# Kernel optimization log

Measured on AMD Instinct MI355X. Metric: run time of the kernel, lower is better.

Reference implementation:

```python
import jax, jax.numpy as jnp
import numpy as np

N, E, G = 20000, 320000, 16
IN, HID, OUT, HEADS = 256, 64, 256, 4
D0 = HID * HEADS  # 256, output dim of layer 0 (concat)


def _p(key, shape, scale=0.05):
    return (jax.random.normal(key, shape, dtype=jnp.float32) * scale)


def setup_inputs() -> dict:
    key = jax.random.key(0)
    ks = jax.random.split(key, 24)
    x = jax.random.normal(ks[0], (N, IN), dtype=jnp.float32)
    edge_index = jax.random.randint(ks[1], (2, E), 0, N, dtype=jnp.int64)
    batch = jnp.sort(jax.random.randint(ks[2], (N,), 0, G, dtype=jnp.int64))
    d = {"x": x, "edge_index": edge_index, "batch": batch}
    # Layer 0: TransformerConv(256 -> 64, heads=4, concat=True, beta=True)
    d["Wq0"] = _p(ks[3], (IN, D0)); d["bq0"] = jnp.zeros((D0,), jnp.float32)
    d["Wk0"] = _p(ks[4], (IN, D0)); d["bk0"] = jnp.zeros((D0,), jnp.float32)
    d["Wv0"] = _p(ks[5], (IN, D0)); d["bv0"] = jnp.zeros((D0,), jnp.float32)
    d["Ws0"] = _p(ks[6], (IN, D0)); d["bs0"] = jnp.zeros((D0,), jnp.float32)
    d["Wb0"] = _p(ks[7], (3 * D0, 1))
    d["g0"] = jnp.ones((D0,), jnp.float32); d["b0"] = jnp.zeros((D0,), jnp.float32)
    # Layer 1: TransformerConv(256 -> 256, heads=1, concat=False, beta=True)
    d["Wq1"] = _p(ks[8], (D0, OUT)); d["bq1"] = jnp.zeros((OUT,), jnp.float32)
    d["Wk1"] = _p(ks[9], (D0, OUT)); d["bk1"] = jnp.zeros((OUT,), jnp.float32)
    d["Wv1"] = _p(ks[10], (D0, OUT)); d["bv1"] = jnp.zeros((OUT,), jnp.float32)
    d["Ws1"] = _p(ks[11], (D0, OUT)); d["bs1"] = jnp.zeros((OUT,), jnp.float32)
    d["Wb1"] = _p(ks[12], (3 * OUT, 1))
    d["g1"] = jnp.ones((OUT,), jnp.float32); d["b1"] = jnp.zeros((OUT,), jnp.float32)
    return d


def _transformer_conv(x, src, dst, Wq, bq, Wk, bk, Wv, bv, Ws, bs, Wb, H, C, concat):
    n = x.shape[0]
    q = (x @ Wq + bq).reshape(n, H, C)
    k = (x @ Wk + bk).reshape(n, H, C)
    v = (x @ Wv + bv).reshape(n, H, C)
    # per-edge attention logits [E, H]
    alpha = (q[dst] * k[src]).sum(-1) / jnp.sqrt(jnp.asarray(C, jnp.float32))
    # segment softmax over incoming edges of each dst node
    m = jax.ops.segment_max(alpha, dst, num_segments=n)  # [N, H]
    a = jnp.exp(alpha - m[dst])
    s = jax.ops.segment_sum(a, dst, num_segments=n)  # [N, H]
    a = a / s[dst]
    out = jax.ops.segment_sum(a[:, :, None] * v[src], dst, num_segments=n)  # [N,H,C]
    out = out.reshape(n, H * C) if concat else out.mean(axis=1)
    # beta-gated skip connection
    r = x @ Ws + bs
    g = jax.nn.sigmoid(jnp.concatenate([out, r, out - r], axis=-1) @ Wb)  # [N,1]
    return g * r + (1.0 - g) * out


def _layer_norm(x, g, b, eps=1e-5):
    mu = x.mean(-1, keepdims=True)
    var = x.var(-1, keepdims=True)
    return (x - mu) * jax.lax.rsqrt(var + eps) * g + b


def reference(x, edge_index, batch,
              Wq0, bq0, Wk0, bk0, Wv0, bv0, Ws0, bs0, Wb0, g0, b0,
              Wq1, bq1, Wk1, bk1, Wv1, bv1, Ws1, bs1, Wb1, g1, b1):
    src, dst = edge_index[0], edge_index[1]
    h = _transformer_conv(x, src, dst, Wq0, bq0, Wk0, bk0, Wv0, bv0, Ws0, bs0, Wb0, HEADS, HID, True)
    h = jax.nn.relu(_layer_norm(h, g0, b0))  # dropout is identity at inference
    h = _transformer_conv(h, src, dst, Wq1, bq1, Wk1, bk1, Wv1, bv1, Ws1, bs1, Wb1, 1, OUT, False)
    h = _layer_norm(h, g1, b1)
    # global mean pool over graphs
    sums = jax.ops.segment_sum(h, batch, num_segments=G)
    counts = jax.ops.segment_sum(jnp.ones((h.shape[0],), h.dtype), batch, num_segments=G)
    return sums / jnp.maximum(counts, 1.0)[:, None]
```

## Files before the change

### kernel.cpp

```cpp
#include <hip/hip_runtime.h>
#include <hip/hip_bf16.h>


#define DEVFN static __device__ __forceinline__

typedef __attribute__((ext_vector_type(4))) float f32x4;
typedef __attribute__((ext_vector_type(2))) float f32x2;
typedef __attribute__((ext_vector_type(8))) short bf16x8;

DEVFN float bfu2f(unsigned short u) {
    union { unsigned int i; float f; } t; t.i = ((unsigned)u) << 16; return t.f;
}
DEVFN float4 ldb4(const __hip_bfloat16* p) {
    ushort4 u = *reinterpret_cast<const ushort4*>(p);
    return make_float4(bfu2f(u.x), bfu2f(u.y), bfu2f(u.z), bfu2f(u.w));
}
DEVFN unsigned short f2bu(float f) {
    __hip_bfloat16 b = __float2bfloat16(f);
    return __builtin_bit_cast(unsigned short, b);
}
DEVFN void stb4(__hip_bfloat16* p, float4 v) {
    ushort4 u;
    u.x = f2bu(v.x); u.y = f2bu(v.y); u.z = f2bu(v.z); u.w = f2bu(v.w);
    *reinterpret_cast<ushort4*>(p) = u;
}
DEVFN float4 f8x4_to_f4(unsigned u) {
    const f32x2 lo = __builtin_amdgcn_cvt_pk_f32_fp8((int)u, false);
    const f32x2 hi = __builtin_amdgcn_cvt_pk_f32_fp8((int)u, true);
    return make_float4(lo.x, lo.y, hi.x, hi.y);
}

DEVFN float dot16(const float* q, uint4 u) {
    const float4 f0 = f8x4_to_f4(u.x);
    const float4 f1 = f8x4_to_f4(u.y);
    const float4 f2 = f8x4_to_f4(u.z);
    const float4 f3 = f8x4_to_f4(u.w);
    float p;
    p = q[0] * f0.x;            p = fmaf(q[1],  f0.y, p);
    p = fmaf(q[2],  f0.z, p);   p = fmaf(q[3],  f0.w, p);
    p = fmaf(q[4],  f1.x, p);   p = fmaf(q[5],  f1.y, p);
    p = fmaf(q[6],  f1.z, p);   p = fmaf(q[7],  f1.w, p);
    p = fmaf(q[8],  f2.x, p);   p = fmaf(q[9],  f2.y, p);
    p = fmaf(q[10], f2.z, p);   p = fmaf(q[11], f2.w, p);
    p = fmaf(q[12], f3.x, p);   p = fmaf(q[13], f3.y, p);
    p = fmaf(q[14], f3.z, p);   p = fmaf(q[15], f3.w, p);
    return p;
}
DEVFN void accum16(float* acc, uint4 u, float a) {
    const float4 f0 = f8x4_to_f4(u.x);
    const float4 f1 = f8x4_to_f4(u.y);
    const float4 f2 = f8x4_to_f4(u.z);
    const float4 f3 = f8x4_to_f4(u.w);
    acc[0]  = fmaf(a, f0.x, acc[0]);  acc[1]  = fmaf(a, f0.y, acc[1]);
    acc[2]  = fmaf(a, f0.z, acc[2]);  acc[3]  = fmaf(a, f0.w, acc[3]);
    acc[4]  = fmaf(a, f1.x, acc[4]);  acc[5]  = fmaf(a, f1.y, acc[5]);
    acc[6]  = fmaf(a, f1.z, acc[6]);  acc[7]  = fmaf(a, f1.w, acc[7]);
    acc[8]  = fmaf(a, f2.x, acc[8]);  acc[9]  = fmaf(a, f2.y, acc[9]);
    acc[10] = fmaf(a, f2.z, acc[10]); acc[11] = fmaf(a, f2.w, acc[11]);
    acc[12] = fmaf(a, f3.x, acc[12]); acc[13] = fmaf(a, f3.y, acc[13]);
    acc[14] = fmaf(a, f3.z, acc[14]); acc[15] = fmaf(a, f3.w, acc[15]);
}

__global__ __launch_bounds__(256)
void f2b_kernel(const float* __restrict__ in, __hip_bfloat16* __restrict__ out, int n4)
{
    const int i = blockIdx.x * 256 + threadIdx.x;
    if (i >= n4) return;
    const float4 v = *reinterpret_cast<const float4*>(in + (size_t)i * 4);
    stb4(out + (size_t)i * 4, v);
}

__global__ __launch_bounds__(256)
void wconv_kernel(const float* __restrict__ W0, const float* __restrict__ W1,
                  const float* __restrict__ W2, const float* __restrict__ W3,
                  const float* __restrict__ W4, const float* __restrict__ W5,
                  const float* __restrict__ W6, const float* __restrict__ W7,
                  __hip_bfloat16* __restrict__ Wt)
{
    const float* W;
    switch (blockIdx.y) {
        case 0: W = W0; break; case 1: W = W1; break;
        case 2: W = W2; break; case 3: W = W3; break;
        case 4: W = W4; break; case 5: W = W5; break;
        case 6: W = W6; break; default: W = W7; break;
    }
    const int k = blockIdx.x;
    const int c = threadIdx.x;
    Wt[(size_t)blockIdx.y * 65536 + (size_t)c * 256 + k] =
        __float2bfloat16(W[(size_t)k * 256 + c]);
}

#define SWZ(r, kb) ((r) * 256 + ((kb) ^ (((r) & 7) << 4)))
#define TSTRIDE 272

__global__ __launch_bounds__(256)
void gemm_mfma_kernel(const __hip_bfloat16* __restrict__ A, int M,
                      const __hip_bfloat16* __restrict__ Wt,
                      const float* __restrict__ b0, const float* __restrict__ b1,
                      const float* __restrict__ b2, const float* __restrict__ b3,
                      void* __restrict__ O0, void* __restrict__ O1,
                      void* __restrict__ O2, void* __restrict__ O3,
                      int s0, int s1, int s2, int s3,
                      int f0, int f1, int f2, int f3)
{
    const int q8   = gridDim.x >> 3;
    const int wgid = (blockIdx.x & 7) * q8 + (blockIdx.x >> 3);
    const int rowblk = wgid >> 3;
    const int rem    = wgid & 7;
    const int colblk = rem >> 2;
    const int z      = rem & 3;

    const float* bias; void* O; int rs, isf8;
    switch (z) {
        case 0:  bias = b0; O = O0; rs = s0; isf8 = f0; break;
        case 1:  bias = b1; O = O1; rs = s1; isf8 = f1; break;
        case 2:  bias = b2; O = O2; rs = s2; isf8 = f2; break;
        default: bias = b3; O = O3; rs = s3; isf8 = f3; break;
    }
    const __hip_bfloat16* Wz = Wt + (size_t)z * 65536;

    __shared__ char Sh[2 * 128 * 256];
    char* As = Sh;
    char* Bs = Sh + 128 * 256;

    const int tid  = threadIdx.x;
    const int row0 = rowblk * 128;
    const int col0 = colblk * 128;
    const int wid  = tid >> 6, lane = tid & 63;
    const int wr   = wid >> 1, wc = wid & 1;
    const int lrow = lane & 15, kg = lane >> 4;

    const int chunk = tid & 15;
    const int rsub  = tid >> 4;

    f32x4 acc[4][4] = {};

    for (int k0 = 0; k0 < 256; k0 += 128) {
        #pragma unroll
        for (int p = 0; p < 8; ++p) {
            const int r  = p * 16 + rsub;
            const int gr = row0 + r;
            ulonglong2 av = {0ull, 0ull};
            if (gr < M)
                av = *reinterpret_cast<const ulonglong2*>(A + (size_t)gr * 256 + k0 + chunk * 8);
            *reinterpret_cast<ulonglong2*>(As + SWZ(r, chunk * 16)) = av;

            const ulonglong2 bv = *reinterpret_cast<const ulonglong2*>(
                Wz + (size_t)(col0 + r) * 256 + k0 + chunk * 8);
            *reinterpret_cast<ulonglong2*>(Bs + SWZ(r, chunk * 16)) = bv;
        }
        __syncthreads();

        #pragma unroll
        for (int kk = 0; kk < 128; kk += 32) {
            const int kbyte = kk * 2 + kg * 16;
            bf16x8 af[4], bfr[4];
            #pragma unroll
            for (int m = 0; m < 4; ++m) {
                const int r = wr * 64 + m * 16 + lrow;
                af[m] = *reinterpret_cast<const bf16x8*>(As + SWZ(r, kbyte));
            }
            #pragma unroll
            for (int n = 0; n < 4; ++n) {
                const int c = wc * 64 + n * 16 + lrow;
                bfr[n] = *reinterpret_cast<const bf16x8*>(Bs + SWZ(c, kbyte));
            }
            #pragma unroll
            for (int m = 0; m < 4; ++m)
                #pragma unroll
                for (int n = 0; n < 4; ++n)
                    acc[m][n] = __builtin_amdgcn_mfma_f32_16x16x32_bf16(
                        af[m], bfr[n], acc[m][n], 0, 0, 0);
        }
        __syncthreads();
    }

    #pragma unroll
    for (int m = 0; m < 4; ++m) {
        #pragma unroll
        for (int j = 0; j < 4; ++j) {
            const int rr = wr * 64 + m * 16 + kg * 4 + j;
            #pragma unroll
            for (int n = 0; n < 4; ++n) {
                const int cc = wc * 64 + n * 16 + lrow;
                const float v = acc[m][n][j] + bias[col0 + cc];
                *reinterpret_cast<unsigned short*>(Sh + rr * TSTRIDE + cc * 2) = f2bu(v);
            }
        }
    }
    __syncthreads();

    const int row  = tid >> 1;
    const int half = tid & 1;
    const int grow = row0 + row;
    if (grow >= M) return;
    const char* src = Sh + row * TSTRIDE + half * 128;

    if (isf8) {
        unsigned char* dst = (unsigned char*)O + (size_t)grow * rs + col0 + half * 64;
        #pragma unroll
        for (int i2 = 0; i2 < 4; ++i2) {
            uint4 w;
            unsigned tmp[4];
            #pragma unroll
            for (int c8 = 0; c8 < 2; ++c8) {
                const bf16x8 e = *reinterpret_cast<const bf16x8*>(src + (i2 * 2 + c8) * 16);
                const int p0 = __builtin_amdgcn_cvt_pk_fp8_f32(
                    bfu2f((unsigned short)e[0]), bfu2f((unsigned short)e[1]), 0, false);
                const int p1 = __builtin_amdgcn_cvt_pk_fp8_f32(
                    bfu2f((unsigned short)e[2]), bfu2f((unsigned short)e[3]), 0, false);
                const int p2 = __builtin_amdgcn_cvt_pk_fp8_f32(
                    bfu2f((unsigned short)e[4]), bfu2f((unsigned short)e[5]), 0, false);
                const int p3 = __builtin_amdgcn_cvt_pk_fp8_f32(
                    bfu2f((unsigned short)e[6]), bfu2f((unsigned short)e[7]), 0, false);
                tmp[c8 * 2 + 0] = (unsigned)(p0 & 0xFFFF) | ((unsigned)(p1 & 0xFFFF) << 16);
                tmp[c8 * 2 + 1] = (unsigned)(p2 & 0xFFFF) | ((unsigned)(p3 & 0xFFFF) << 16);
            }
            w.x = tmp[0]; w.y = tmp[1]; w.z = tmp[2]; w.w = tmp[3];
            *reinterpret_cast<uint4*>(dst + i2 * 16) = w;
        }
    } else {
        char* dst = (char*)((__hip_bfloat16*)O + (size_t)grow * rs + col0 + half * 64);
        #pragma unroll
        for (int i = 0; i < 8; ++i)
            *reinterpret_cast<ulonglong2*>(dst + i * 16) =
                *reinterpret_cast<const ulonglong2*>(src + i * 16);
    }
}

__global__ __launch_bounds__(256)
void hist_kernel(const int* __restrict__ ei, int E, int* __restrict__ deg)
{
    const int e = blockIdx.x * 256 + threadIdx.x;
    if (e < E) atomicAdd(&deg[ei[E + e]], 1);
}

__global__ __launch_bounds__(256)
void gcount_kernel(const int* __restrict__ batch, int N, int* __restrict__ gcount)
{
    __shared__ int h[16];
    if (threadIdx.x < 16) h[threadIdx.x] = 0;
    __syncthreads();
    const int n = blockIdx.x * 256 + threadIdx.x;
    if (n < N) atomicAdd(&h[batch[n]], 1);
    __syncthreads();
    if (threadIdx.x < 16 && h[threadIdx.x] != 0)
        atomicAdd(&gcount[threadIdx.x], h[threadIdx.x]);
}

__global__ __launch_bounds__(64)
void gstart_kernel(const int* __restrict__ gcount, int* __restrict__ gstart)
{
    if (threadIdx.x == 0) {
        int o = 0;
        for (int g = 0; g < 16; ++g) { gstart[g] = o; o += gcount[g]; }
        gstart[16] = o;
    }
}

__global__ __launch_bounds__(1024)
void scan_kernel(const int* __restrict__ deg, int* __restrict__ row_start, int n)
{
    __shared__ int wsum[16];
    __shared__ int wincl[16];
    const int tid  = threadIdx.x;
    const int w    = tid >> 6;
    const int lane = tid & 63;
    if (tid == 0) row_start[0] = 0;
    int offset = 0;
    for (int base = 0; base < n; base += 1024) {
        const int idx = base + tid;
        int s = (idx < n) ? deg[idx] : 0;
        #pragma unroll
        for (int d = 1; d < 64; d <<= 1) {
            const int t = __shfl_up(s, d, 64);
            if (lane >= d) s += t;
        }
        if (lane == 63) wsum[w] = s;
        __syncthreads();
        if (tid < 16) {
            int si = wsum[tid];
            #pragma unroll
            for (int d = 1; d < 16; d <<= 1) {
                const int u = __shfl_up(si, d, 64);
                if (tid >= d) si += u;
            }
            wincl[tid] = si;
        }
        __syncthreads();
        const int woff = (w > 0) ? wincl[w - 1] : 0;
        if (idx < n) row_start[idx + 1] = offset + woff + s;
        offset += wincl[15];
        __syncthreads();
    }
}

__global__ __launch_bounds__(256)
void fill_kernel(const int* __restrict__ ei, int E,
                 const int* __restrict__ row_start,
                 int* __restrict__ cursor, int* __restrict__ csr_src)
{
    const int e = blockIdx.x * 256 + threadIdx.x;
    if (e >= E) return;
    const int s = ei[e];
    const int d = ei[E + e];
    const int pos = atomicAdd(&cursor[d], 1);
    csr_src[row_start[d] + pos] = s;
}

template <int NSH, bool RELU, bool OUTB>
__global__ __launch_bounds__(256)
void attn_kernel(const __hip_bfloat16* __restrict__ Q,
                 const unsigned char* __restrict__ KV,
                 const __hip_bfloat16* __restrict__ R,
                 const float* __restrict__ Wb, const float* __restrict__ lng,
                 const float* __restrict__ lnb,
                 const int* __restrict__ row_start, const int* __restrict__ csr_src,
                 __hip_bfloat16* __restrict__ outb, float* __restrict__ outf,
                 int N, float scale)
{
    const int wv   = threadIdx.x >> 6;
    const int lane = threadIdx.x & 63;
    const int g    = lane >> 4;
    const int s    = lane & 15;
    const int node = blockIdx.x * 4 + wv;
    if (node >= N) return;

    float q[16];
    {
        const bf16x8 a = *reinterpret_cast<const bf16x8*>(Q + (size_t)node * 256 + s * 16);
        const bf16x8 b = *reinterpret_cast<const bf16x8*>(Q + (size_t)node * 256 + s * 16 + 8);
        #pragma unroll
        for (int j = 0; j < 8; ++j) {
            q[j]     = bfu2f((unsigned short)a[j]);
            q[8 + j] = bfu2f((unsigned short)b[j]);
        }
    }

    const int beg = row_start[node];
    const int end = row_start[node + 1];

    float acc[16] = {};
    float ssum = 0.f;

    int i = beg + g;
    for (; i + 4 < end; i += 8) {
        const int sa = csr_src[i];
        const int sb = csr_src[i + 4];
        const uint4 ka = *reinterpret_cast<const uint4*>(KV + (size_t)sa * 512 + s * 16);
        const uint4 va = *reinterpret_cast<const uint4*>(KV + (size_t)sa * 512 + 256 + s * 16);
        const uint4 kb = *reinterpret_cast<const uint4*>(KV + (size_t)sb * 512 + s * 16);
        const uint4 vb = *reinterpret_cast<const uint4*>(KV + (size_t)sb * 512 + 256 + s * 16);
        float pa = dot16(q, ka);
        float pb = dot16(q, kb);
        #pragma unroll
        for (int m = 1; m < (1 << NSH); m <<= 1) {
            pa += __shfl_xor(pa, m, 64);
            pb += __shfl_xor(pb, m, 64);
        }
        const float aa = __expf(pa * scale);
        const float ab = __expf(pb * scale);
        ssum += aa + ab;
        accum16(acc, va, aa);
        accum16(acc, vb, ab);
    }
    if (i < end) {
        const int sa = csr_src[i];
        const uint4 ka = *reinterpret_cast<const uint4*>(KV + (size_t)sa * 512 + s * 16);
        const uint4 va = *reinterpret_cast<const uint4*>(KV + (size_t)sa * 512 + 256 + s * 16);
        float pa = dot16(q, ka);
        #pragma unroll
        for (int m = 1; m < (1 << NSH); m <<= 1) pa += __shfl_xor(pa, m, 64);
        const float aa = __expf(pa * scale);
        ssum += aa;
        accum16(acc, va, aa);
    }

    ssum += __shfl_xor(ssum, 16, 64);
    ssum += __shfl_xor(ssum, 32, 64);
    #pragma unroll
    for (int j = 0; j < 16; ++j) {
        acc[j] += __shfl_xor(acc[j], 16, 64);
        acc[j] += __shfl_xor(acc[j], 32, 64);
    }

    if (g != 0) return;

    const float is = (ssum > 0.f) ? 1.f / ssum : 0.f;
    float o[16];
    #pragma unroll
    for (int j = 0; j < 16; ++j) o[j] = acc[j] * is;

    float r[16];
    {
        const bf16x8 a = *reinterpret_cast<const bf16x8*>(R + (size_t)node * 256 + s * 16);
        const bf16x8 b = *reinterpret_cast<const bf16x8*>(R + (size_t)node * 256 + s * 16 + 8);
        #pragma unroll
        for (int j = 0; j < 8; ++j) {
            r[j]     = bfu2f((unsigned short)a[j]);
            r[8 + j] = bfu2f((unsigned short)b[j]);
        }
    }

    float z = 0.f;
    #pragma unroll
    for (int j = 0; j < 16; ++j) {
        const int d = s * 16 + j;
        z += o[j] * Wb[d] + r[j] * Wb[256 + d] + (o[j] - r[j]) * Wb[512 + d];
    }
    #pragma unroll
    for (int m = 1; m < 16; m <<= 1) z += __shfl_xor(z, m, 64);
    const float gg = 1.f / (1.f + __expf(-z));

    float h[16];
    float s1 = 0.f, s2 = 0.f;
    #pragma unroll
    for (int j = 0; j < 16; ++j) {
        h[j] = gg * r[j] + (1.f - gg) * o[j];
        s1 += h[j];
        s2 += h[j] * h[j];
    }
    #pragma unroll
    for (int m = 1; m < 16; m <<= 1) {
        s1 += __shfl_xor(s1, m, 64);
        s2 += __shfl_xor(s2, m, 64);
    }
    const float mu  = s1 * (1.f / 256.f);
    const float var = s2 * (1.f / 256.f) - mu * mu;
    const float inv = rsqrtf(var + 1e-5f);

    #pragma unroll
    for (int j = 0; j < 16; ++j) {
        const int d = s * 16 + j;
        h[j] = (h[j] - mu) * inv * lng[d] + lnb[d];
        if (RELU) h[j] = fmaxf(h[j], 0.f);
    }

    if (OUTB) {
        __hip_bfloat16* dst = outb + (size_t)node * 256 + s * 16;
        stb4(dst,      make_float4(h[0],  h[1],  h[2],  h[3]));
        stb4(dst + 4,  make_float4(h[4],  h[5],  h[6],  h[7]));
        stb4(dst + 8,  make_float4(h[8],  h[9],  h[10], h[11]));
        stb4(dst + 12, make_float4(h[12], h[13], h[14], h[15]));
    } else {
        float* dst = outf + (size_t)node * 256 + s * 16;
        #pragma unroll
        for (int c4 = 0; c4 < 4; ++c4)
            *reinterpret_cast<float4*>(dst + c4 * 4) =
                make_float4(h[c4 * 4], h[c4 * 4 + 1], h[c4 * 4 + 2], h[c4 * 4 + 3]);
    }
}

__global__ __launch_bounds__(256)
void pool_partial_kernel(const float* __restrict__ h, const int* __restrict__ gstart,
                         float* __restrict__ partial)
{
    const int s    = blockIdx.x;
    const int g    = blockIdx.y;
    const int tid  = threadIdx.x;
    const int quad = tid & 63;
    const int sub  = tid >> 6;

    const int beg = gstart[g];
    const int cnt = gstart[g + 1] - beg;

    f32x4 acc = {0.f, 0.f, 0.f, 0.f};
    for (int i = s * 4 + sub; i < cnt; i += 64) {
        const f32x4 v = *reinterpret_cast<const f32x4*>(
            h + (size_t)(beg + i) * 256 + quad * 4);
        acc += v;
    }

    __shared__ f32x4 sh[4][64];
    sh[sub][quad] = acc;
    __syncthreads();
    if (sub == 0) {
        const f32x4 r = sh[0][quad] + sh[1][quad] + sh[2][quad] + sh[3][quad];
        *reinterpret_cast<f32x4*>(partial + ((size_t)(g * 16 + s) * 64 + quad) * 4) = r;
    }
}

__global__ __launch_bounds__(256)
void pool_final_kernel(const float* __restrict__ partial, const int* __restrict__ gcount,
                       float* __restrict__ out)
{
    const int g = blockIdx.x;
    const int d = threadIdx.x;
    float sum = 0.f;
    #pragma unroll
    for (int s = 0; s < 16; ++s)
        sum += partial[(size_t)(g * 16 + s) * 256 + d];
    out[(size_t)g * 256 + d] = sum / (float)max(gcount[g], 1);
}

extern "C" void kernel_launch(void* const* d_in, const int* in_sizes, int n_in,
                              void* d_out, int out_size, void* d_ws, size_t ws_size,
                              hipStream_t stream)
{
    const float* x     = (const float*)d_in[0];
    const int*   ei    = (const int*)d_in[1];
    const int*   batch = (const int*)d_in[2];
    const float* Wq0 = (const float*)d_in[3];  const float* bq0 = (const float*)d_in[4];
    const float* Wk0 = (const float*)d_in[5];  const float* bk0 = (const float*)d_in[6];
    const float* Wv0 = (const float*)d_in[7];  const float* bv0 = (const float*)d_in[8];
    const float* Ws0 = (const float*)d_in[9];  const float* bs0 = (const float*)d_in[10];
    const float* Wb0 = (const float*)d_in[11];
    const float* g0  = (const float*)d_in[12]; const float* b0  = (const float*)d_in[13];
    const float* Wq1 = (const float*)d_in[14]; const float* bq1 = (const float*)d_in[15];
    const float* Wk1 = (const float*)d_in[16]; const float* bk1 = (const float*)d_in[17];
    const float* Wv1 = (const float*)d_in[18]; const float* bv1 = (const float*)d_in[19];
    const float* Ws1 = (const float*)d_in[20]; const float* bs1 = (const float*)d_in[21];
    const float* Wb1 = (const float*)d_in[22];
    const float* g1  = (const float*)d_in[23]; const float* b1  = (const float*)d_in[24];

    const int N = in_sizes[0] / 256;
    const int E = in_sizes[1] / 2;
    const int G = 16;
    const size_t NM = (size_t)N * 256;

    __hip_bfloat16* bws = (__hip_bfloat16*)d_ws;
    __hip_bfloat16* xb  = bws;
    __hip_bfloat16* qb  = xb  + NM;
    __hip_bfloat16* rb  = qb  + NM;
    __hip_bfloat16* h0b = rb  + NM;
    __hip_bfloat16* wt  = h0b + NM;
    unsigned char* kvb  = (unsigned char*)(wt + 8 * 65536);
    float* h1f     = (float*)(kvb + (size_t)N * 512);
    float* partial = h1f + NM;
    int* deg       = (int*)(partial + 16 * 16 * 256);
    int* row_start = deg + N;
    int* cursor    = row_start + N + 1;
    int* gcount    = cursor + N;
    int* gstart    = gcount + G;
    int* csr_src   = gstart + 17;

    const size_t zbytes = ((size_t)N + (N + 1) + N + G + 17) * sizeof(int);
    hipMemsetAsync(deg, 0, zbytes, stream);

    const int eb = (E + 255) / 256;
    const int nb = (N + 255) / 256;

    f2b_kernel<<<(int)((NM / 4 + 255) / 256), 256, 0, stream>>>(x, xb, (int)(NM / 4));
    wconv_kernel<<<dim3(256, 8), 256, 0, stream>>>(Wq0, Wk0, Wv0, Ws0,
                                                   Wq1, Wk1, Wv1, Ws1, wt);

    hist_kernel<<<eb, 256, 0, stream>>>(ei, E, deg);
    gcount_kernel<<<nb, 256, 0, stream>>>(batch, N, gcount);
    gstart_kernel<<<1, 64, 0, stream>>>(gcount, gstart);
    scan_kernel<<<1, 1024, 0, stream>>>(deg, row_start, N);
    fill_kernel<<<eb, 256, 0, stream>>>(ei, E, row_start, cursor, csr_src);

    const int nrb   = (N + 127) / 128;
    const int ggrid = nrb * 8;
    const int agrid = (N + 3) / 4;

    gemm_mfma_kernel<<<ggrid, 256, 0, stream>>>(xb, N, wt,
        bq0, bk0, bv0, bs0,
        qb, kvb, kvb + 256, rb,
        256, 512, 512, 256,
        0, 1, 1, 0);
    attn_kernel<2, true, true><<<agrid, 256, 0, stream>>>(
        qb, kvb, rb, Wb0, g0, b0, row_start, csr_src, h0b, nullptr, N, 0.125f);

    gemm_mfma_kernel<<<ggrid, 256, 0, stream>>>(h0b, N, wt + 4 * 65536,
        bq1, bk1, bv1, bs1,
        qb, kvb, kvb + 256, rb,
        256, 512, 512, 256,
        0, 1, 1, 0);
    attn_kernel<4, false, false><<<agrid, 256, 0, stream>>>(
        qb, kvb, rb, Wb1, g1, b1, row_start, csr_src, nullptr, h1f, N, 0.0625f);

    pool_partial_kernel<<<dim3(16, 16), 256, 0, stream>>>(h1f, gstart, partial);
    pool_final_kernel<<<16, 256, 0, stream>>>(partial, gcount, (float*)d_out);
}
```

Baseline: 235.3 us.

## Merge prep and graph-build kernels and unroll attention edge loop by four

The float-to-bf16 input conversion and the weight transpose/convert kernels are merged into a single launch, and so are the degree histogram and graph-count kernels, which removes two kernel launches and their gaps. Separately, the attention gather loop now handles four edges per iteration instead of two, so more independent K/V loads are in flight to hide gather latency. The tail becomes a loop over the remaining edges. The wider unroll raises register pressure and may lower occupancy.

```diff
diff --git a/kernel.cpp b/kernel.cpp
--- a/kernel.cpp
+++ b/kernel.cpp
@@ -10,10 +10,6 @@
 
 DEVFN float bfu2f(unsigned short u) {
     union { unsigned int i; float f; } t; t.i = ((unsigned)u) << 16; return t.f;
-}
-DEVFN float4 ldb4(const __hip_bfloat16* p) {
-    ushort4 u = *reinterpret_cast<const ushort4*>(p);
-    return make_float4(bfu2f(u.x), bfu2f(u.y), bfu2f(u.z), bfu2f(u.w));
 }
 DEVFN unsigned short f2bu(float f) {
     __hip_bfloat16 b = __float2bfloat16(f);
@@ -62,32 +58,33 @@
 }
 
 __global__ __launch_bounds__(256)
-void f2b_kernel(const float* __restrict__ in, __hip_bfloat16* __restrict__ out, int n4)
-{
-    const int i = blockIdx.x * 256 + threadIdx.x;
-    if (i >= n4) return;
-    const float4 v = *reinterpret_cast<const float4*>(in + (size_t)i * 4);
-    stb4(out + (size_t)i * 4, v);
-}
-
-__global__ __launch_bounds__(256)
-void wconv_kernel(const float* __restrict__ W0, const float* __restrict__ W1,
-                  const float* __restrict__ W2, const float* __restrict__ W3,
-                  const float* __restrict__ W4, const float* __restrict__ W5,
-                  const float* __restrict__ W6, const float* __restrict__ W7,
-                  __hip_bfloat16* __restrict__ Wt)
-{
-    const float* W;
-    switch (blockIdx.y) {
-        case 0: W = W0; break; case 1: W = W1; break;
-        case 2: W = W2; break; case 3: W = W3; break;
-        case 4: W = W4; break; case 5: W = W5; break;
-        case 6: W = W6; break; default: W = W7; break;
-    }
-    const int k = blockIdx.x;
-    const int c = threadIdx.x;
-    Wt[(size_t)blockIdx.y * 65536 + (size_t)c * 256 + k] =
-        __float2bfloat16(W[(size_t)k * 256 + c]);
+void prep_kernel(const float* __restrict__ x, __hip_bfloat16* __restrict__ xb, int nf2b,
+                 const float* __restrict__ W0, const float* __restrict__ W1,
+                 const float* __restrict__ W2, const float* __restrict__ W3,
+                 const float* __restrict__ W4, const float* __restrict__ W5,
+                 const float* __restrict__ W6, const float* __restrict__ W7,
+                 __hip_bfloat16* __restrict__ Wt)
+{
+    const int b = blockIdx.x;
+    if (b < nf2b) {
+        const int i = b * 256 + threadIdx.x;
+        const float4 v = *reinterpret_cast<const float4*>(x + (size_t)i * 4);
+        stb4(xb + (size_t)i * 4, v);
+    } else {
+        const int wb = b - nf2b;
+        const int z  = wb >> 8;
+        const int k  = wb & 255;
+        const int c  = threadIdx.x;
+        const float* W;
+        switch (z) {
+            case 0: W = W0; break; case 1: W = W1; break;
+            case 2: W = W2; break; case 3: W = W3; break;
+            case 4: W = W4; break; case 5: W = W5; break;
+            case 6: W = W6; break; default: W = W7; break;
+        }
+        Wt[(size_t)z * 65536 + (size_t)c * 256 + k] =
+            __float2bfloat16(W[(size_t)k * 256 + c]);
+    }
 }
 
 #define SWZ(r, kb) ((r) * 256 + ((kb) ^ (((r) & 7) << 4)))
@@ -229,23 +226,22 @@
 }
 
 __global__ __launch_bounds__(256)
-void hist_kernel(const int* __restrict__ ei, int E, int* __restrict__ deg)
-{
-    const int e = blockIdx.x * 256 + threadIdx.x;
-    if (e < E) atomicAdd(&deg[ei[E + e]], 1);
-}
-
-__global__ __launch_bounds__(256)
-void gcount_kernel(const int* __restrict__ batch, int N, int* __restrict__ gcount)
-{
-    __shared__ int h[16];
-    if (threadIdx.x < 16) h[threadIdx.x] = 0;
-    __syncthreads();
-    const int n = blockIdx.x * 256 + threadIdx.x;
-    if (n < N) atomicAdd(&h[batch[n]], 1);
-    __syncthreads();
-    if (threadIdx.x < 16 && h[threadIdx.x] != 0)
-        atomicAdd(&gcount[threadIdx.x], h[threadIdx.x]);
+void build_kernel(const int* __restrict__ ei, int E, int* __restrict__ deg, int nhist,
+                  const int* __restrict__ batch, int N, int* __restrict__ gcount)
+{
+    if (blockIdx.x < nhist) {
+        const int e = blockIdx.x * 256 + threadIdx.x;
+        if (e < E) atomicAdd(&deg[ei[E + e]], 1);
+    } else {
+        __shared__ int h[16];
+        if (threadIdx.x < 16) h[threadIdx.x] = 0;
+        __syncthreads();
+        const int n = (blockIdx.x - nhist) * 256 + threadIdx.x;
+        if (n < N) atomicAdd(&h[batch[n]], 1);
+        __syncthreads();
+        if (threadIdx.x < 16 && h[threadIdx.x] != 0)
+            atomicAdd(&gcount[threadIdx.x], h[threadIdx.x]);
+    }
 }
 
 __global__ __launch_bounds__(64)
@@ -344,27 +340,41 @@
     float ssum = 0.f;
 
     int i = beg + g;
-    for (; i + 4 < end; i += 8) {
-        const int sa = csr_src[i];
-        const int sb = csr_src[i + 4];
-        const uint4 ka = *reinterpret_cast<const uint4*>(KV + (size_t)sa * 512 + s * 16);
-        const uint4 va = *reinterpret_cast<const uint4*>(KV + (size_t)sa * 512 + 256 + s * 16);
-        const uint4 kb = *reinterpret_cast<const uint4*>(KV + (size_t)sb * 512 + s * 16);
-        const uint4 vb = *reinterpret_cast<const uint4*>(KV + (size_t)sb * 512 + 256 + s * 16);
-        float pa = dot16(q, ka);
-        float pb = dot16(q, kb);
+    for (; i + 12 < end; i += 16) {
+        const int s0 = csr_src[i];
+        const int s1 = csr_src[i + 4];
+        const int s2 = csr_src[i + 8];
+        const int s3 = csr_src[i + 12];
+        const uint4 k0 = *reinterpret_cast<const uint4*>(KV + (size_t)s0 * 512 + s * 16);
+        const uint4 v0 = *reinterpret_cast<const uint4*>(KV + (size_t)s0 * 512 + 256 + s * 16);
+        const uint4 k1 = *reinterpret_cast<const uint4*>(KV + (size_t)s1 * 512 + s * 16);
+        const uint4 v1 = *reinterpret_cast<const uint4*>(KV + (size_t)s1 * 512 + 256 + s * 16);
+        const uint4 k2 = *reinterpret_cast<const uint4*>(KV + (size_t)s2 * 512 + s * 16);
+        const uint4 v2 = *reinterpret_cast<const uint4*>(KV + (size_t)s2 * 512 + 256 + s * 16);
+        const uint4 k3 = *reinterpret_cast<const uint4*>(KV + (size_t)s3 * 512 + s * 16);
+        const uint4 v3 = *reinterpret_cast<const uint4*>(KV + (size_t)s3 * 512 + 256 + s * 16);
+        float p0 = dot16(q, k0);
+        float p1 = dot16(q, k1);
+        float p2 = dot16(q, k2);
+        float p3 = dot16(q, k3);
         #pragma unroll
         for (int m = 1; m < (1 << NSH); m <<= 1) {
-            pa += __shfl_xor(pa, m, 64);
-            pb += __shfl_xor(pb, m, 64);
-        }
-        const float aa = __expf(pa * scale);
-        const float ab = __expf(pb * scale);
-        ssum += aa + ab;
-        accum16(acc, va, aa);
-        accum16(acc, vb, ab);
-    }
-    if (i < end) {
+            p0 += __shfl_xor(p0, m, 64);
+            p1 += __shfl_xor(p1, m, 64);
+            p2 += __shfl_xor(p2, m, 64);
+            p3 += __shfl_xor(p3, m, 64);
+        }
+        const float a0 = __expf(p0 * scale);
+        const float a1 = __expf(p1 * scale);
+        const float a2 = __expf(p2 * scale);
+        const float a3 = __expf(p3 * scale);
+        ssum += (a0 + a1) + (a2 + a3);
+        accum16(acc, v0, a0);
+        accum16(acc, v1, a1);
+        accum16(acc, v2, a2);
+        accum16(acc, v3, a3);
+    }
+    for (; i < end; i += 4) {
         const int sa = csr_src[i];
         const uint4 ka = *reinterpret_cast<const uint4*>(KV + (size_t)sa * 512 + s * 16);
         const uint4 va = *reinterpret_cast<const uint4*>(KV + (size_t)sa * 512 + 256 + s * 16);
@@ -539,13 +549,12 @@
 
     const int eb = (E + 255) / 256;
     const int nb = (N + 255) / 256;
-
-    f2b_kernel<<<(int)((NM / 4 + 255) / 256), 256, 0, stream>>>(x, xb, (int)(NM / 4));
-    wconv_kernel<<<dim3(256, 8), 256, 0, stream>>>(Wq0, Wk0, Wv0, Ws0,
-                                                   Wq1, Wk1, Wv1, Ws1, wt);
-
-    hist_kernel<<<eb, 256, 0, stream>>>(ei, E, deg);
-    gcount_kernel<<<nb, 256, 0, stream>>>(batch, N, gcount);
+    const int nf2b = (int)((NM / 4 + 255) / 256);
+
+    prep_kernel<<<nf2b + 2048, 256, 0, stream>>>(x, xb, nf2b,
+        Wq0, Wk0, Wv0, Ws0, Wq1, Wk1, Wv1, Ws1, wt);
+
+    build_kernel<<<eb + nb, 256, 0, stream>>>(ei, E, deg, eb, batch, N, gcount);
     gstart_kernel<<<1, 64, 0, stream>>>(gcount, gstart);
     scan_kernel<<<1, 1024, 0, stream>>>(deg, row_start, N);
     fill_kernel<<<eb, 256, 0, stream>>>(ei, E, row_start, cursor, csr_src);
```

Measured after the change: 239.5 us. No clear change (+1.8%).

## Fuse fp32-to-bf16 conversion into GEMM, merge setup kernels, shrink attention blocks

Applied to the files above, without the earlier changes.

The first GEMM now reads the fp32 input directly and converts it to bf16 while staging tiles in shared memory, so the separate conversion kernel and its bf16 buffer are gone. The histogram and graph-count kernels are merged into one launch, and the graph-start prefix is folded into the scan kernel, which cuts three launches. The attention kernels now use 128-thread blocks with two nodes per block instead of 256 threads and four nodes. The GEMM reads twice as many bytes for A in the first layer, and the smaller attention blocks change occupancy and scheduling granularity.

```diff
diff --git a/kernel.cpp b/kernel.cpp
--- a/kernel.cpp
+++ b/kernel.cpp
@@ -10,10 +10,6 @@
 
 DEVFN float bfu2f(unsigned short u) {
     union { unsigned int i; float f; } t; t.i = ((unsigned)u) << 16; return t.f;
-}
-DEVFN float4 ldb4(const __hip_bfloat16* p) {
-    ushort4 u = *reinterpret_cast<const ushort4*>(p);
-    return make_float4(bfu2f(u.x), bfu2f(u.y), bfu2f(u.z), bfu2f(u.w));
 }
 DEVFN unsigned short f2bu(float f) {
     __hip_bfloat16 b = __float2bfloat16(f);
@@ -62,15 +58,6 @@
 }
 
 __global__ __launch_bounds__(256)
-void f2b_kernel(const float* __restrict__ in, __hip_bfloat16* __restrict__ out, int n4)
-{
-    const int i = blockIdx.x * 256 + threadIdx.x;
-    if (i >= n4) return;
-    const float4 v = *reinterpret_cast<const float4*>(in + (size_t)i * 4);
-    stb4(out + (size_t)i * 4, v);
-}
-
-__global__ __launch_bounds__(256)
 void wconv_kernel(const float* __restrict__ W0, const float* __restrict__ W1,
                   const float* __restrict__ W2, const float* __restrict__ W3,
                   const float* __restrict__ W4, const float* __restrict__ W5,
@@ -93,8 +80,9 @@
 #define SWZ(r, kb) ((r) * 256 + ((kb) ^ (((r) & 7) << 4)))
 #define TSTRIDE 272
 
+template <bool AF32>
 __global__ __launch_bounds__(256)
-void gemm_mfma_kernel(const __hip_bfloat16* __restrict__ A, int M,
+void gemm_mfma_kernel(const void* __restrict__ Av, int M,
                       const __hip_bfloat16* __restrict__ Wt,
                       const float* __restrict__ b0, const float* __restrict__ b1,
                       const float* __restrict__ b2, const float* __restrict__ b3,
@@ -140,10 +128,28 @@
         for (int p = 0; p < 8; ++p) {
             const int r  = p * 16 + rsub;
             const int gr = row0 + r;
-            ulonglong2 av = {0ull, 0ull};
-            if (gr < M)
-                av = *reinterpret_cast<const ulonglong2*>(A + (size_t)gr * 256 + k0 + chunk * 8);
-            *reinterpret_cast<ulonglong2*>(As + SWZ(r, chunk * 16)) = av;
+
+            if (AF32) {
+                const float* Af = (const float*)Av;
+                ushort4 lo = {0, 0, 0, 0}, hi = {0, 0, 0, 0};
+                if (gr < M) {
+                    const float4 a = *reinterpret_cast<const float4*>(
+                        Af + (size_t)gr * 256 + k0 + chunk * 8);
+                    const float4 b = *reinterpret_cast<const float4*>(
+                        Af + (size_t)gr * 256 + k0 + chunk * 8 + 4);
+                    lo.x = f2bu(a.x); lo.y = f2bu(a.y); lo.z = f2bu(a.z); lo.w = f2bu(a.w);
+                    hi.x = f2bu(b.x); hi.y = f2bu(b.y); hi.z = f2bu(b.z); hi.w = f2bu(b.w);
+                }
+                *reinterpret_cast<ushort4*>(As + SWZ(r, chunk * 16))     = lo;
+                *reinterpret_cast<ushort4*>(As + SWZ(r, chunk * 16) + 8) = hi;
+            } else {
+                const __hip_bfloat16* Ab = (const __hip_bfloat16*)Av;
+                ulonglong2 av = {0ull, 0ull};
+                if (gr < M)
+                    av = *reinterpret_cast<const ulonglong2*>(
+                        Ab + (size_t)gr * 256 + k0 + chunk * 8);
+                *reinterpret_cast<ulonglong2*>(As + SWZ(r, chunk * 16)) = av;
+            }
 
             const ulonglong2 bv = *reinterpret_cast<const ulonglong2*>(
                 Wz + (size_t)(col0 + r) * 256 + k0 + chunk * 8);
@@ -229,44 +235,40 @@
 }
 
 __global__ __launch_bounds__(256)
-void hist_kernel(const int* __restrict__ ei, int E, int* __restrict__ deg)
-{
-    const int e = blockIdx.x * 256 + threadIdx.x;
-    if (e < E) atomicAdd(&deg[ei[E + e]], 1);
-}
-
-__global__ __launch_bounds__(256)
-void gcount_kernel(const int* __restrict__ batch, int N, int* __restrict__ gcount)
-{
-    __shared__ int h[16];
-    if (threadIdx.x < 16) h[threadIdx.x] = 0;
-    __syncthreads();
-    const int n = blockIdx.x * 256 + threadIdx.x;
-    if (n < N) atomicAdd(&h[batch[n]], 1);
-    __syncthreads();
-    if (threadIdx.x < 16 && h[threadIdx.x] != 0)
-        atomicAdd(&gcount[threadIdx.x], h[threadIdx.x]);
-}
-
-__global__ __launch_bounds__(64)
-void gstart_kernel(const int* __restrict__ gcount, int* __restrict__ gstart)
-{
-    if (threadIdx.x == 0) {
-        int o = 0;
-        for (int g = 0; g < 16; ++g) { gstart[g] = o; o += gcount[g]; }
-        gstart[16] = o;
+void build_kernel(const int* __restrict__ ei, int E, int* __restrict__ deg, int nhist,
+                  const int* __restrict__ batch, int N, int* __restrict__ gcount)
+{
+    if (blockIdx.x < nhist) {
+        const int e = blockIdx.x * 256 + threadIdx.x;
+        if (e < E) atomicAdd(&deg[ei[E + e]], 1);
+    } else {
+        __shared__ int h[16];
+        if (threadIdx.x < 16) h[threadIdx.x] = 0;
+        __syncthreads();
+        const int n = (blockIdx.x - nhist) * 256 + threadIdx.x;
+        if (n < N) atomicAdd(&h[batch[n]], 1);
+        __syncthreads();
+        if (threadIdx.x < 16 && h[threadIdx.x] != 0)
+            atomicAdd(&gcount[threadIdx.x], h[threadIdx.x]);
     }
 }
 
 __global__ __launch_bounds__(1024)
-void scan_kernel(const int* __restrict__ deg, int* __restrict__ row_start, int n)
+void scan_kernel(const int* __restrict__ deg, int* __restrict__ row_start, int n,
+                 const int* __restrict__ gcount, int* __restrict__ gstart)
 {
     __shared__ int wsum[16];
     __shared__ int wincl[16];
     const int tid  = threadIdx.x;
     const int w    = tid >> 6;
     const int lane = tid & 63;
-    if (tid == 0) row_start[0] = 0;
+    if (tid == 0) {
+        row_start[0] = 0;
+        int o = 0;
+        #pragma unroll
+        for (int g = 0; g < 16; ++g) { gstart[g] = o; o += gcount[g]; }
+        gstart[16] = o;
+    }
     int offset = 0;
     for (int base = 0; base < n; base += 1024) {
         const int idx = base + tid;
@@ -309,7 +311,7 @@
 }
 
 template <int NSH, bool RELU, bool OUTB>
-__global__ __launch_bounds__(256)
+__global__ __launch_bounds__(128)
 void attn_kernel(const __hip_bfloat16* __restrict__ Q,
                  const unsigned char* __restrict__ KV,
                  const __hip_bfloat16* __restrict__ R,
@@ -323,7 +325,7 @@
     const int lane = threadIdx.x & 63;
     const int g    = lane >> 4;
     const int s    = lane & 15;
-    const int node = blockIdx.x * 4 + wv;
+    const int node = blockIdx.x * 2 + wv;
     if (node >= N) return;
 
     float q[16];
@@ -519,8 +521,7 @@
     const size_t NM = (size_t)N * 256;
 
     __hip_bfloat16* bws = (__hip_bfloat16*)d_ws;
-    __hip_bfloat16* xb  = bws;
-    __hip_bfloat16* qb  = xb  + NM;
+    __hip_bfloat16* qb  = bws;
     __hip_bfloat16* rb  = qb  + NM;
     __hip_bfloat16* h0b = rb  + NM;
     __hip_bfloat16* wt  = h0b + NM;
@@ -540,34 +541,31 @@
     const int eb = (E + 255) / 256;
     const int nb = (N + 255) / 256;
 
-    f2b_kernel<<<(int)((NM / 4 + 255) / 256), 256, 0, stream>>>(x, xb, (int)(NM / 4));
     wconv_kernel<<<dim3(256, 8), 256, 0, stream>>>(Wq0, Wk0, Wv0, Ws0,
                                                    Wq1, Wk1, Wv1, Ws1, wt);
 
-    hist_kernel<<<eb, 256, 0, stream>>>(ei, E, deg);
-    gcount_kernel<<<nb, 256, 0, stream>>>(batch, N, gcount);
-    gstart_kernel<<<1, 64, 0, stream>>>(gcount, gstart);
-    scan_kernel<<<1, 1024, 0, stream>>>(deg, row_start, N);
+    build_kernel<<<eb + nb, 256, 0, stream>>>(ei, E, deg, eb, batch, N, gcount);
+    scan_kernel<<<1, 1024, 0, stream>>>(deg, row_start, N, gcount, gstart);
     fill_kernel<<<eb, 256, 0, stream>>>(ei, E, row_start, cursor, csr_src);
 
     const int nrb   = (N + 127) / 128;
     const int ggrid = nrb * 8;
-    const int agrid = (N + 3) / 4;
-
-    gemm_mfma_kernel<<<ggrid, 256, 0, stream>>>(xb, N, wt,
+    const int agrid = (N + 1) / 2;
+
+    gemm_mfma_kernel<true><<<ggrid, 256, 0, stream>>>(x, N, wt,
         bq0, bk0, bv0, bs0,
         qb, kvb, kvb + 256, rb,
         256, 512, 512, 256,
         0, 1, 1, 0);
-    attn_kernel<2, true, true><<<agrid, 256, 0, stream>>>(
+    attn_kernel<2, true, true><<<agrid, 128, 0, stream>>>(
         qb, kvb, rb, Wb0, g0, b0, row_start, csr_src, h0b, nullptr, N, 0.125f);
 
-    gemm_mfma_kernel<<<ggrid, 256, 0, stream>>>(h0b, N, wt + 4 * 65536,
+    gemm_mfma_kernel<false><<<ggrid, 256, 0, stream>>>(h0b, N, wt + 4 * 65536,
         bq1, bk1, bv1, bs1,
         qb, kvb, kvb + 256, rb,
         256, 512, 512, 256,
         0, 1, 1, 0);
-    attn_kernel<4, false, false><<<agrid, 256, 0, stream>>>(
+    attn_kernel<4, false, false><<<agrid, 128, 0, stream>>>(
         qb, kvb, rb, Wb1, g1, b1, row_start, csr_src, nullptr, h1f, N, 0.0625f);
 
     pool_partial_kernel<<<dim3(16, 16), 256, 0, stream>>>(h1f, gstart, partial);
```

New measurement: 235.3 us. Within noise of the previous version (-0.0%).
